# Kernel optimization log

Measured on AMD Instinct MI355X. Metric: run time of the kernel, lower is better.

The kernel has to match this reference:

```python
import jax, jax.numpy as jnp
import numpy as np


def setup_inputs() -> dict:
    key = jax.random.key(0)
    k1, k2, k3, k4 = jax.random.split(key, 4)
    B, C, H, W = 8, 3, 1024, 2048
    M, h, w = 32, H // 8, W // 8
    img = jax.random.uniform(k1, (B, C, H, W), dtype=jnp.float32)
    planar_masks = jax.random.normal(k2, (B, M, h, w), dtype=jnp.float32)
    disp = jax.random.uniform(k3, (B, h, w), dtype=jnp.float32) * 0.9 + 0.1
    K = jnp.array([[721.5, 0.0, w / 2.0], [0.0, 721.5, h / 2.0], [0.0, 0.0, 1.0]], dtype=jnp.float32)
    intrs = jnp.tile(K[None], (B, 1, 1))
    baseline = jax.random.uniform(k4, (B,), dtype=jnp.float32) * 0.4 + 0.3
    return {"img": img, "planar_masks": planar_masks, "disp": disp, "intrs": intrs, "baseline": baseline}


def reference(img, planar_masks, disp, intrs, baseline):
    B, C, H, W = img.shape
    _, M, h, w = planar_masks.shape
    dt = img.dtype

    # disp -> depth (b,h,w)
    focal = (intrs[:, 0, 0] + intrs[:, 1, 1]) * 0.5
    depth = baseline[:, None, None] * focal[:, None, None] / (disp * 2048.0)

    # depth -> normals via 3x3 Sobel-style central differences, zero padding
    dp = jnp.pad(depth, ((0, 0), (1, 1), (1, 1)))
    gx = 0.5 * (dp[:, 1:-1, 2:] - dp[:, 1:-1, :-2])
    gy = 0.5 * (dp[:, 2:, 1:-1] - dp[:, :-2, 1:-1])
    dir_map = jnp.stack([-gx, -gy, jnp.ones_like(gx)], axis=1)  # (B,3,h,w)
    normal = dir_map / jnp.sqrt(jnp.sum(dir_map ** 2, axis=1, keepdims=True))

    # softmax-weighted per-plane depth/normal (faithful torch .view memory layout)
    wts = jax.nn.softmax(planar_masks.reshape(B, M, h * w), axis=-1)  # (B,M,hw)
    flat_depth = depth.reshape(B, h * w, 1)
    flat_normal = normal.reshape(B, h * w, 3)  # channel-major flatten, as in source
    planar_depth = wts @ flat_depth   # (B,M,1)
    planar_normal = wts @ flat_normal  # (B,M,3)

    # per-plane homographies H = K (R - t n^T / d) K^-1
    R = jnp.broadcast_to(jnp.eye(3, dtype=dt), (B, 3, 3))
    t = jnp.zeros((B, 3, 1), dt).at[:, 2, 0].set(-baseline)
    K_inv = jnp.linalg.inv(intrs)
    tn = t[:, None] @ planar_normal[:, :, None, :]            # (B,M,3,3)
    H_cal = R[:, None] - tn / planar_depth[..., None]
    Hm = intrs[:, None] @ H_cal @ K_inv[:, None]              # (B,M,3,3)

    img_p = img.reshape(B, C, h, 8, w, 8).mean(axis=(3, 5))  # (B,C,h,w)

    # affine_grid (align_corners=True) with the top 2 rows of H
    ys = jnp.linspace(-1.0, 1.0, h, dtype=dt)
    xs = jnp.linspace(-1.0, 1.0, w, dtype=dt)
    gyy, gxx = jnp.meshgrid(ys, xs, indexing="ij")
    base = jnp.stack([gxx, gyy, jnp.ones_like(gxx)], axis=-1)  # (h,w,3)
    grid = jnp.einsum("bmij,hwj->bmhwi", Hm[:, :, :2, :], base)  # (B,M,h,w,2)

    # bilinear grid_sample, zeros padding, align_corners=True
    ix = (grid[..., 0] + 1.0) * (w - 1) * 0.5
    iy = (grid[..., 1] + 1.0) * (h - 1) * 0.5
    x0 = jnp.floor(ix)
    y0 = jnp.floor(iy)
    wx1 = ix - x0
    wy1 = iy - y0
    imgT = img_p.transpose(0, 2, 3, 1)  # (B,h,w,C)
    bidx = jnp.arange(B)[:, None, None, None]

    def corner(xf, yf):
        valid = (xf >= 0) & (xf <= w - 1) & (yf >= 0) & (yf <= h - 1)
        xi = jnp.clip(xf, 0, w - 1).astype(jnp.int32)
        yi = jnp.clip(yf, 0, h - 1).astype(jnp.int32)
        return imgT[bidx, yi, xi] * valid[..., None].astype(dt)  # (B,M,h,w,C)

    warp = (corner(x0, y0) * ((1 - wx1) * (1 - wy1))[..., None]
            + corner(x0 + 1, y0) * (wx1 * (1 - wy1))[..., None]
            + corner(x0, y0 + 1) * ((1 - wx1) * wy1)[..., None]
            + corner(x0 + 1, y0 + 1) * (wx1 * wy1)[..., None])  # (B,M,h,w,C)

    blend = jax.nn.softmax(planar_masks, axis=1)  # (B,M,h,w)
    return jnp.einsum("bmhwc,bmhw->bchw", warp, blend)
```

## Files before the change

kernel.cpp:

```cpp
#include <hip/hip_runtime.h>
#include <math.h>

#define Bq   8
#define Cc   3
#define Hh   128
#define Ww   256
#define Mm   32
#define HW   (Hh*Ww)
#define HIMG 1024
#define WIMG 2048

__global__ void k_pool_dn(const float* __restrict__ img,
                          float4* __restrict__ img_p,
                          const float* __restrict__ disp,
                          const float* __restrict__ intrs,
                          const float* __restrict__ baseline,
                          float* __restrict__ depth,
                          float* __restrict__ normal) {
    int blk = blockIdx.x;
    if (blk < Bq * Hh) {
        int b = blk >> 7, y = blk & (Hh - 1);
        int x = threadIdx.x;
        float s[3];
        #pragma unroll
        for (int c = 0; c < 3; c++) {
            const float* base = img + ((size_t)(b * 3 + c) * HIMG + (size_t)y * 8) * WIMG + x * 8;
            float acc = 0.f;
            #pragma unroll
            for (int r = 0; r < 8; r++) {
                float4 u = *(const float4*)(base + (size_t)r * WIMG);
                float4 v = *(const float4*)(base + (size_t)r * WIMG + 4);
                acc += u.x + u.y + u.z + u.w + v.x + v.y + v.z + v.w;
            }
            s[c] = acc * (1.0f / 64.0f);
        }
        img_p[(size_t)blk * Ww + x] = make_float4(s[0], s[1], s[2], 0.f);
    } else {
        int idx = (blk - Bq * Hh) * 256 + threadIdx.x;
        int b = idx >> 15;
        int p = idx & (HW - 1);
        int y = p >> 8;
        int x = p & (Ww - 1);
        float focal = 0.5f * (intrs[b * 9 + 0] + intrs[b * 9 + 4]);
        float k = baseline[b] * focal * (1.0f / 2048.0f);
        const float* db = disp + (size_t)b * HW;
        float Dc  = k / db[p];
        float Dxm = (x > 0)      ? k / db[p - 1]  : 0.0f;
        float Dxp = (x < Ww - 1) ? k / db[p + 1]  : 0.0f;
        float Dym = (y > 0)      ? k / db[p - Ww] : 0.0f;
        float Dyp = (y < Hh - 1) ? k / db[p + Ww] : 0.0f;
        float gx = 0.5f * (Dxp - Dxm);
        float gy = 0.5f * (Dyp - Dym);
        float invn = 1.0f / sqrtf(gx * gx + gy * gy + 1.0f);
        depth[idx] = Dc;
        float* nb = normal + (size_t)b * 3 * HW;
        nb[p]          = -gx * invn;
        nb[HW + p]     = -gy * invn;
        nb[2 * HW + p] =  invn;
    }
}

__global__ __launch_bounds__(1024) void k_planes(
        const float* __restrict__ masks,
        const float* __restrict__ depth,
        const float* __restrict__ normal,
        const float* __restrict__ intrs,
        const float* __restrict__ baseline,
        float* __restrict__ hm) {
    __shared__ float lds[5][16];
    int bm = blockIdx.x;
    int b = bm >> 5;
    const float4* mp = (const float4*)(masks + (size_t)bm * HW);
    const float4* dp = (const float4*)(depth + (size_t)b * HW);
    const float4* np = (const float4*)(normal + (size_t)b * 3 * HW);
    int tid = threadIdx.x;
    int lane = tid & 63, wid = tid >> 6;

    float se = 0.f, sd = 0.f, s0 = 0.f, s1 = 0.f, s2 = 0.f;
    #pragma unroll 4
    for (int kk = 0; kk < HW / 4 / 1024; kk++) {
        int i = tid + kk * 1024;
        float4 mk  = mp[i];
        float4 d4  = dp[i];
        float4 n0v = np[3 * i], n1v = np[3 * i + 1], n2v = np[3 * i + 2];
        float e0 = __expf(mk.x), e1 = __expf(mk.y);
        float e2 = __expf(mk.z), e3 = __expf(mk.w);
        se += (e0 + e1) + (e2 + e3);
        sd = fmaf(e0, d4.x, fmaf(e1, d4.y, fmaf(e2, d4.z, fmaf(e3, d4.w, sd))));
        s0 = fmaf(e0, n0v.x, fmaf(e1, n0v.w, fmaf(e2, n1v.z, fmaf(e3, n2v.y, s0))));
        s1 = fmaf(e0, n0v.y, fmaf(e1, n1v.x, fmaf(e2, n1v.w, fmaf(e3, n2v.z, s1))));
        s2 = fmaf(e0, n0v.z, fmaf(e1, n1v.y, fmaf(e2, n2v.x, fmaf(e3, n2v.w, s2))));
    }
    float vals[5] = {se, sd, s0, s1, s2};
    #pragma unroll
    for (int j = 0; j < 5; j++) {
        float v = vals[j];
        #pragma unroll
        for (int off = 32; off; off >>= 1) v += __shfl_down(v, off, 64);
        if (lane == 0) lds[j][wid] = v;
    }
    __syncthreads();

    if (tid == 0) {
        float t[5];
        #pragma unroll
        for (int j = 0; j < 5; j++) {
            float r = 0.f;
            #pragma unroll
            for (int i = 0; i < 16; i++) r += lds[j][i];
            t[j] = r;
        }
        float inv_se = 1.0f / t[0];
        float pd = t[1] * inv_se;
        float n0 = t[2] * inv_se, n1 = t[3] * inv_se, n2 = t[4] * inv_se;
        const float* Km = intrs + b * 9;
        float a = Km[0], bb = Km[1], c = Km[2];
        float d = Km[3], e  = Km[4], f = Km[5];
        float g = Km[6], h2 = Km[7], i = Km[8];
        float det = a * (e * i - f * h2) - bb * (d * i - f * g) + c * (d * h2 - e * g);
        float invd = 1.0f / det;
        float ki[9] = {(e * i - f * h2) * invd, (c * h2 - bb * i) * invd, (bb * f - c * e) * invd,
                       (f * g - d * i) * invd, (a * i - c * g) * invd,  (c * d - a * f) * invd,
                       (d * h2 - e * g) * invd, (bb * g - a * h2) * invd, (a * e - bb * d) * invd};
        float s = baseline[b] / pd;
        float A[9] = {1.f, 0.f, 0.f, 0.f, 1.f, 0.f, s * n0, s * n1, 1.0f + s * n2};
        float T[9];
        #pragma unroll
        for (int r = 0; r < 3; r++)
            #pragma unroll
            for (int cc = 0; cc < 3; cc++)
                T[r * 3 + cc] = Km[r * 3 + 0] * A[cc] + Km[r * 3 + 1] * A[3 + cc] + Km[r * 3 + 2] * A[6 + cc];
        #pragma unroll
        for (int r = 0; r < 2; r++)
            #pragma unroll
            for (int cc = 0; cc < 3; cc++)
                hm[bm * 6 + r * 3 + cc] = T[r * 3 + 0] * ki[cc] + T[r * 3 + 1] * ki[3 + cc] + T[r * 3 + 2] * ki[6 + cc];
    }
}

__global__ void k_blend(const float* __restrict__ masks,
                        const float* __restrict__ hm,
                        const float4* __restrict__ img_p,
                        float* __restrict__ out) {
    int bi = blockIdx.x;
    int b = bi >> 7;
    int y = bi & (Hh - 1);
    int x = threadIdx.x;
    __shared__ float hs[Mm * 6];
    if (x < Mm * 6) hs[x] = hm[b * Mm * 6 + x];
    __syncthreads();

    const float* mp = masks + (size_t)b * Mm * HW + (size_t)y * Ww + x;
    float mv[Mm];
    #pragma unroll
    for (int m = 0; m < Mm; m++) mv[m] = mp[(size_t)m * HW];

    float xn = (2.0f * x - (float)(Ww - 1)) * (1.0f / (float)(Ww - 1));
    float yn = (2.0f * y - (float)(Hh - 1)) * (1.0f / (float)(Hh - 1));
    const float4* ip = img_p + (size_t)b * HW;

    float se = 0.f, a0 = 0.f, a1 = 0.f, a2 = 0.f;
    #pragma unroll 4
    for (int m = 0; m < Mm; m++) {
        float e = __expf(mv[m]);
        se += e;
        float gx = fmaf(hs[m * 6 + 0], xn, fmaf(hs[m * 6 + 1], yn, hs[m * 6 + 2]));
        float gy = fmaf(hs[m * 6 + 3], xn, fmaf(hs[m * 6 + 4], yn, hs[m * 6 + 5]));
        float ix = (gx + 1.0f) * ((float)(Ww - 1) * 0.5f);
        float iy = (gy + 1.0f) * ((float)(Hh - 1) * 0.5f);
        float x0f = floorf(ix), y0f = floorf(iy);
        float wx1 = ix - x0f, wy1 = iy - y0f;
        float wx0 = 1.0f - wx1, wy0 = 1.0f - wy1;
        float w00 = wx0 * wy0 * e, w10 = wx1 * wy0 * e;
        float w01 = wx0 * wy1 * e, w11 = wx1 * wy1 * e;
        #define CORNER(xf, yf, wt) do {                                              \
            float _xf = (xf), _yf = (yf);                                            \
            bool _v = (_xf >= 0.0f) && (_xf <= (float)(Ww - 1)) &&                   \
                      (_yf >= 0.0f) && (_yf <= (float)(Hh - 1));                     \
            float _xc = fminf(fmaxf(_xf, 0.0f), (float)(Ww - 1));                    \
            float _yc = fminf(fmaxf(_yf, 0.0f), (float)(Hh - 1));                    \
            int _o = (int)_yc * Ww + (int)_xc;                                       \
            float4 _t = ip[_o];                                                      \
            float _w = _v ? (wt) : 0.0f;                                             \
            a0 = fmaf(_w, _t.x, a0);                                                 \
            a1 = fmaf(_w, _t.y, a1);                                                 \
            a2 = fmaf(_w, _t.z, a2);                                                 \
        } while (0)
        CORNER(x0f,        y0f,        w00);
        CORNER(x0f + 1.0f, y0f,        w10);
        CORNER(x0f,        y0f + 1.0f, w01);
        CORNER(x0f + 1.0f, y0f + 1.0f, w11);
        #undef CORNER
    }
    float inv = 1.0f / se;
    int o = y * Ww + x;
    float* ob = out + (size_t)b * 3 * HW;
    ob[o]          = a0 * inv;
    ob[HW + o]     = a1 * inv;
    ob[2 * HW + o] = a2 * inv;
}

extern "C" void kernel_launch(void* const* d_in, const int* in_sizes, int n_in,
                              void* d_out, int out_size, void* d_ws, size_t ws_size,
                              hipStream_t stream) {
    const float* img      = (const float*)d_in[0];
    const float* masks    = (const float*)d_in[1];
    const float* disp     = (const float*)d_in[2];
    const float* intrs    = (const float*)d_in[3];
    const float* baseline = (const float*)d_in[4];
    float* out = (float*)d_out;

    float* depth  = (float*)d_ws;
    float* normal = depth + (size_t)Bq * HW;
    float* hm     = normal + (size_t)Bq * 3 * HW;
    float4* img_p = (float4*)(hm + (size_t)Bq * Mm * 6);

    hipLaunchKernelGGL(k_pool_dn, dim3(2 * Bq * Hh), dim3(256), 0, stream,
                       img, img_p, disp, intrs, baseline, depth, normal);
    hipLaunchKernelGGL(k_planes, dim3(Bq * Mm), dim3(1024), 0, stream,
                       masks, depth, normal, intrs, baseline, hm);
    hipLaunchKernelGGL(k_blend, dim3(Bq * Hh), dim3(256), 0, stream,
                       masks, hm, img_p, out);
}
```

Before: 339.0 us.

## Overlap image pooling with plane reduction and split blend planes across two halves

Depth/normal computation moves into its own small kernel, and the large image pooling now runs in the same launch as the per-plane softmax reductions, so the two bandwidth-heavy phases can overlap instead of pooling sharing a launch with the tiny depth work. The plane reduction drops to 512 threads per block. The blend kernel uses 512 threads per row, with each half handling 16 of the 32 planes, and combines the partial sums through shared memory. This raises parallelism and lowers register pressure. The bilinear validity test is also simplified to per-axis unsigned compares. The cost is extra shared memory and a second sync in blend.

```diff
diff --git a/kernel.cpp b/kernel.cpp
--- a/kernel.cpp
+++ b/kernel.cpp
@@ -10,17 +10,116 @@
 #define HIMG 1024
 #define WIMG 2048
 
-__global__ void k_pool_dn(const float* __restrict__ img,
-                          float4* __restrict__ img_p,
-                          const float* __restrict__ disp,
-                          const float* __restrict__ intrs,
-                          const float* __restrict__ baseline,
-                          float* __restrict__ depth,
-                          float* __restrict__ normal) {
+__global__ void k_dn(const float* __restrict__ disp,
+                     const float* __restrict__ intrs,
+                     const float* __restrict__ baseline,
+                     float* __restrict__ depth,
+                     float* __restrict__ normal) {
+    int idx = blockIdx.x * 256 + threadIdx.x;
+    int b = idx >> 15;
+    int p = idx & (HW - 1);
+    int y = p >> 8;
+    int x = p & (Ww - 1);
+    float focal = 0.5f * (intrs[b * 9 + 0] + intrs[b * 9 + 4]);
+    float k = baseline[b] * focal * (1.0f / 2048.0f);
+    const float* db = disp + (size_t)b * HW;
+    float Dc  = k / db[p];
+    float Dxm = (x > 0)      ? k / db[p - 1]  : 0.0f;
+    float Dxp = (x < Ww - 1) ? k / db[p + 1]  : 0.0f;
+    float Dym = (y > 0)      ? k / db[p - Ww] : 0.0f;
+    float Dyp = (y < Hh - 1) ? k / db[p + Ww] : 0.0f;
+    float gx = 0.5f * (Dxp - Dxm);
+    float gy = 0.5f * (Dyp - Dym);
+    float invn = 1.0f / sqrtf(gx * gx + gy * gy + 1.0f);
+    depth[idx] = Dc;
+    float* nb = normal + (size_t)b * 3 * HW;
+    nb[p]          = -gx * invn;
+    nb[HW + p]     = -gy * invn;
+    nb[2 * HW + p] =  invn;
+}
+
+__global__ __launch_bounds__(512) void k_pool_planes(
+        const float* __restrict__ img, float4* __restrict__ img_p,
+        const float* __restrict__ masks,
+        const float* __restrict__ depth, const float* __restrict__ normal,
+        const float* __restrict__ intrs, const float* __restrict__ baseline,
+        float* __restrict__ hm) {
     int blk = blockIdx.x;
-    if (blk < Bq * Hh) {
-        int b = blk >> 7, y = blk & (Hh - 1);
-        int x = threadIdx.x;
+    int tid = threadIdx.x;
+    __shared__ float lds[5][8];
+    if (blk < Bq * Mm) {
+        int bm = blk;
+        int b = bm >> 5;
+        const float4* mp = (const float4*)(masks + (size_t)bm * HW);
+        const float4* dp = (const float4*)(depth + (size_t)b * HW);
+        const float4* np = (const float4*)(normal + (size_t)b * 3 * HW);
+        int lane = tid & 63, wid = tid >> 6;
+
+        float se = 0.f, sd = 0.f, s0 = 0.f, s1 = 0.f, s2 = 0.f;
+        #pragma unroll 4
+        for (int kk = 0; kk < HW / 4 / 512; kk++) {
+            int i = tid + kk * 512;
+            float4 mk  = mp[i];
+            float4 d4  = dp[i];
+            float4 n0v = np[3 * i], n1v = np[3 * i + 1], n2v = np[3 * i + 2];
+            float e0 = __expf(mk.x), e1 = __expf(mk.y);
+            float e2 = __expf(mk.z), e3 = __expf(mk.w);
+            se += (e0 + e1) + (e2 + e3);
+            sd = fmaf(e0, d4.x, fmaf(e1, d4.y, fmaf(e2, d4.z, fmaf(e3, d4.w, sd))));
+            s0 = fmaf(e0, n0v.x, fmaf(e1, n0v.w, fmaf(e2, n1v.z, fmaf(e3, n2v.y, s0))));
+            s1 = fmaf(e0, n0v.y, fmaf(e1, n1v.x, fmaf(e2, n1v.w, fmaf(e3, n2v.z, s1))));
+            s2 = fmaf(e0, n0v.z, fmaf(e1, n1v.y, fmaf(e2, n2v.x, fmaf(e3, n2v.w, s2))));
+        }
+        float vals[5] = {se, sd, s0, s1, s2};
+        #pragma unroll
+        for (int j = 0; j < 5; j++) {
+            float v = vals[j];
+            #pragma unroll
+            for (int off = 32; off; off >>= 1) v += __shfl_down(v, off, 64);
+            if (lane == 0) lds[j][wid] = v;
+        }
+        __syncthreads();
+
+        if (tid == 0) {
+            float t[5];
+            #pragma unroll
+            for (int j = 0; j < 5; j++) {
+                float r = 0.f;
+                #pragma unroll
+                for (int i = 0; i < 8; i++) r += lds[j][i];
+                t[j] = r;
+            }
+            float inv_se = 1.0f / t[0];
+            float pd = t[1] * inv_se;
+            float n0 = t[2] * inv_se, n1 = t[3] * inv_se, n2 = t[4] * inv_se;
+            const float* Km = intrs + b * 9;
+            float a = Km[0], bb = Km[1], c = Km[2];
+            float d = Km[3], e  = Km[4], f = Km[5];
+            float g = Km[6], h2 = Km[7], i = Km[8];
+            float det = a * (e * i - f * h2) - bb * (d * i - f * g) + c * (d * h2 - e * g);
+            float invd = 1.0f / det;
+            float ki[9] = {(e * i - f * h2) * invd, (c * h2 - bb * i) * invd, (bb * f - c * e) * invd,
+                           (f * g - d * i) * invd, (a * i - c * g) * invd,  (c * d - a * f) * invd,
+                           (d * h2 - e * g) * invd, (bb * g - a * h2) * invd, (a * e - bb * d) * invd};
+            float s = baseline[b] / pd;
+            float A[9] = {1.f, 0.f, 0.f, 0.f, 1.f, 0.f, s * n0, s * n1, 1.0f + s * n2};
+            float T[9];
+            #pragma unroll
+            for (int r = 0; r < 3; r++)
+                #pragma unroll
+                for (int cc = 0; cc < 3; cc++)
+                    T[r * 3 + cc] = Km[r * 3 + 0] * A[cc] + Km[r * 3 + 1] * A[3 + cc] + Km[r * 3 + 2] * A[6 + cc];
+            #pragma unroll
+            for (int r = 0; r < 2; r++)
+                #pragma unroll
+                for (int cc = 0; cc < 3; cc++)
+                    hm[bm * 6 + r * 3 + cc] = T[r * 3 + 0] * ki[cc] + T[r * 3 + 1] * ki[3 + cc] + T[r * 3 + 2] * ki[6 + cc];
+        }
+    } else {
+        int pb = blk - Bq * Mm;
+        int b = pb >> 6;
+        int y = ((pb & 63) << 1) | (tid >> 8);
+        int x = tid & 255;
         float s[3];
         #pragma unroll
         for (int c = 0; c < 3; c++) {
@@ -34,170 +133,80 @@
             }
             s[c] = acc * (1.0f / 64.0f);
         }
-        img_p[(size_t)blk * Ww + x] = make_float4(s[0], s[1], s[2], 0.f);
-    } else {
-        int idx = (blk - Bq * Hh) * 256 + threadIdx.x;
-        int b = idx >> 15;
-        int p = idx & (HW - 1);
-        int y = p >> 8;
-        int x = p & (Ww - 1);
-        float focal = 0.5f * (intrs[b * 9 + 0] + intrs[b * 9 + 4]);
-        float k = baseline[b] * focal * (1.0f / 2048.0f);
-        const float* db = disp + (size_t)b * HW;
-        float Dc  = k / db[p];
-        float Dxm = (x > 0)      ? k / db[p - 1]  : 0.0f;
-        float Dxp = (x < Ww - 1) ? k / db[p + 1]  : 0.0f;
-        float Dym = (y > 0)      ? k / db[p - Ww] : 0.0f;
-        float Dyp = (y < Hh - 1) ? k / db[p + Ww] : 0.0f;
-        float gx = 0.5f * (Dxp - Dxm);
-        float gy = 0.5f * (Dyp - Dym);
-        float invn = 1.0f / sqrtf(gx * gx + gy * gy + 1.0f);
-        depth[idx] = Dc;
-        float* nb = normal + (size_t)b * 3 * HW;
-        nb[p]          = -gx * invn;
-        nb[HW + p]     = -gy * invn;
-        nb[2 * HW + p] =  invn;
-    }
-}
-
-__global__ __launch_bounds__(1024) void k_planes(
-        const float* __restrict__ masks,
-        const float* __restrict__ depth,
-        const float* __restrict__ normal,
-        const float* __restrict__ intrs,
-        const float* __restrict__ baseline,
-        float* __restrict__ hm) {
-    __shared__ float lds[5][16];
-    int bm = blockIdx.x;
-    int b = bm >> 5;
-    const float4* mp = (const float4*)(masks + (size_t)bm * HW);
-    const float4* dp = (const float4*)(depth + (size_t)b * HW);
-    const float4* np = (const float4*)(normal + (size_t)b * 3 * HW);
-    int tid = threadIdx.x;
-    int lane = tid & 63, wid = tid >> 6;
-
-    float se = 0.f, sd = 0.f, s0 = 0.f, s1 = 0.f, s2 = 0.f;
-    #pragma unroll 4
-    for (int kk = 0; kk < HW / 4 / 1024; kk++) {
-        int i = tid + kk * 1024;
-        float4 mk  = mp[i];
-        float4 d4  = dp[i];
-        float4 n0v = np[3 * i], n1v = np[3 * i + 1], n2v = np[3 * i + 2];
-        float e0 = __expf(mk.x), e1 = __expf(mk.y);
-        float e2 = __expf(mk.z), e3 = __expf(mk.w);
-        se += (e0 + e1) + (e2 + e3);
-        sd = fmaf(e0, d4.x, fmaf(e1, d4.y, fmaf(e2, d4.z, fmaf(e3, d4.w, sd))));
-        s0 = fmaf(e0, n0v.x, fmaf(e1, n0v.w, fmaf(e2, n1v.z, fmaf(e3, n2v.y, s0))));
-        s1 = fmaf(e0, n0v.y, fmaf(e1, n1v.x, fmaf(e2, n1v.w, fmaf(e3, n2v.z, s1))));
-        s2 = fmaf(e0, n0v.z, fmaf(e1, n1v.y, fmaf(e2, n2v.x, fmaf(e3, n2v.w, s2))));
-    }
-    float vals[5] = {se, sd, s0, s1, s2};
-    #pragma unroll
-    for (int j = 0; j < 5; j++) {
-        float v = vals[j];
-        #pragma unroll
-        for (int off = 32; off; off >>= 1) v += __shfl_down(v, off, 64);
-        if (lane == 0) lds[j][wid] = v;
-    }
-    __syncthreads();
-
-    if (tid == 0) {
-        float t[5];
-        #pragma unroll
-        for (int j = 0; j < 5; j++) {
-            float r = 0.f;
-            #pragma unroll
-            for (int i = 0; i < 16; i++) r += lds[j][i];
-            t[j] = r;
-        }
-        float inv_se = 1.0f / t[0];
-        float pd = t[1] * inv_se;
-        float n0 = t[2] * inv_se, n1 = t[3] * inv_se, n2 = t[4] * inv_se;
-        const float* Km = intrs + b * 9;
-        float a = Km[0], bb = Km[1], c = Km[2];
-        float d = Km[3], e  = Km[4], f = Km[5];
-        float g = Km[6], h2 = Km[7], i = Km[8];
-        float det = a * (e * i - f * h2) - bb * (d * i - f * g) + c * (d * h2 - e * g);
-        float invd = 1.0f / det;
-        float ki[9] = {(e * i - f * h2) * invd, (c * h2 - bb * i) * invd, (bb * f - c * e) * invd,
-                       (f * g - d * i) * invd, (a * i - c * g) * invd,  (c * d - a * f) * invd,
-                       (d * h2 - e * g) * invd, (bb * g - a * h2) * invd, (a * e - bb * d) * invd};
-        float s = baseline[b] / pd;
-        float A[9] = {1.f, 0.f, 0.f, 0.f, 1.f, 0.f, s * n0, s * n1, 1.0f + s * n2};
-        float T[9];
-        #pragma unroll
-        for (int r = 0; r < 3; r++)
-            #pragma unroll
-            for (int cc = 0; cc < 3; cc++)
-                T[r * 3 + cc] = Km[r * 3 + 0] * A[cc] + Km[r * 3 + 1] * A[3 + cc] + Km[r * 3 + 2] * A[6 + cc];
-        #pragma unroll
-        for (int r = 0; r < 2; r++)
-            #pragma unroll
-            for (int cc = 0; cc < 3; cc++)
-                hm[bm * 6 + r * 3 + cc] = T[r * 3 + 0] * ki[cc] + T[r * 3 + 1] * ki[3 + cc] + T[r * 3 + 2] * ki[6 + cc];
-    }
-}
-
-__global__ void k_blend(const float* __restrict__ masks,
+        img_p[((size_t)(b * Hh + y)) * Ww + x] = make_float4(s[0], s[1], s[2], 0.f);
+    }
+}
+
+__global__ __launch_bounds__(512) void k_blend(const float* __restrict__ masks,
                         const float* __restrict__ hm,
                         const float4* __restrict__ img_p,
                         float* __restrict__ out) {
     int bi = blockIdx.x;
     int b = bi >> 7;
     int y = bi & (Hh - 1);
-    int x = threadIdx.x;
+    int tid = threadIdx.x;
+    int x = tid & (Ww - 1);
+    int half = tid >> 8;
     __shared__ float hs[Mm * 6];
-    if (x < Mm * 6) hs[x] = hm[b * Mm * 6 + x];
+    __shared__ float part[4][Ww];
+    if (tid < Mm * 6) hs[tid] = hm[b * Mm * 6 + tid];
     __syncthreads();
 
-    const float* mp = masks + (size_t)b * Mm * HW + (size_t)y * Ww + x;
-    float mv[Mm];
+    const float* mp = masks + (size_t)b * Mm * HW + (size_t)(half * 16) * HW
+                    + (size_t)y * Ww + x;
+    float mv[16];
     #pragma unroll
-    for (int m = 0; m < Mm; m++) mv[m] = mp[(size_t)m * HW];
+    for (int m = 0; m < 16; m++) mv[m] = mp[(size_t)m * HW];
 
     float xn = (2.0f * x - (float)(Ww - 1)) * (1.0f / (float)(Ww - 1));
     float yn = (2.0f * y - (float)(Hh - 1)) * (1.0f / (float)(Hh - 1));
     const float4* ip = img_p + (size_t)b * HW;
+    const float* hb = hs + half * 16 * 6;
 
     float se = 0.f, a0 = 0.f, a1 = 0.f, a2 = 0.f;
     #pragma unroll 4
-    for (int m = 0; m < Mm; m++) {
+    for (int m = 0; m < 16; m++) {
         float e = __expf(mv[m]);
         se += e;
-        float gx = fmaf(hs[m * 6 + 0], xn, fmaf(hs[m * 6 + 1], yn, hs[m * 6 + 2]));
-        float gy = fmaf(hs[m * 6 + 3], xn, fmaf(hs[m * 6 + 4], yn, hs[m * 6 + 5]));
+        float gx = fmaf(hb[m * 6 + 0], xn, fmaf(hb[m * 6 + 1], yn, hb[m * 6 + 2]));
+        float gy = fmaf(hb[m * 6 + 3], xn, fmaf(hb[m * 6 + 4], yn, hb[m * 6 + 5]));
         float ix = (gx + 1.0f) * ((float)(Ww - 1) * 0.5f);
         float iy = (gy + 1.0f) * ((float)(Hh - 1) * 0.5f);
         float x0f = floorf(ix), y0f = floorf(iy);
         float wx1 = ix - x0f, wy1 = iy - y0f;
         float wx0 = 1.0f - wx1, wy0 = 1.0f - wy1;
-        float w00 = wx0 * wy0 * e, w10 = wx1 * wy0 * e;
-        float w01 = wx0 * wy1 * e, w11 = wx1 * wy1 * e;
-        #define CORNER(xf, yf, wt) do {                                              \
-            float _xf = (xf), _yf = (yf);                                            \
-            bool _v = (_xf >= 0.0f) && (_xf <= (float)(Ww - 1)) &&                   \
-                      (_yf >= 0.0f) && (_yf <= (float)(Hh - 1));                     \
-            float _xc = fminf(fmaxf(_xf, 0.0f), (float)(Ww - 1));                    \
-            float _yc = fminf(fmaxf(_yf, 0.0f), (float)(Hh - 1));                    \
-            int _o = (int)_yc * Ww + (int)_xc;                                       \
-            float4 _t = ip[_o];                                                      \
-            float _w = _v ? (wt) : 0.0f;                                             \
-            a0 = fmaf(_w, _t.x, a0);                                                 \
-            a1 = fmaf(_w, _t.y, a1);                                                 \
-            a2 = fmaf(_w, _t.z, a2);                                                 \
-        } while (0)
-        CORNER(x0f,        y0f,        w00);
-        CORNER(x0f + 1.0f, y0f,        w10);
-        CORNER(x0f,        y0f + 1.0f, w01);
-        CORNER(x0f + 1.0f, y0f + 1.0f, w11);
-        #undef CORNER
-    }
-    float inv = 1.0f / se;
-    int o = y * Ww + x;
-    float* ob = out + (size_t)b * 3 * HW;
-    ob[o]          = a0 * inv;
-    ob[HW + o]     = a1 * inv;
-    ob[2 * HW + o] = a2 * inv;
+        int x0i = (int)x0f, y0i = (int)y0f;
+        float vx0 = ((unsigned)x0i       < (unsigned)Ww) ? wx0 : 0.0f;
+        float vx1 = ((unsigned)(x0i + 1) < (unsigned)Ww) ? wx1 : 0.0f;
+        float vy0 = ((unsigned)y0i       < (unsigned)Hh) ? wy0 * e : 0.0f;
+        float vy1 = ((unsigned)(y0i + 1) < (unsigned)Hh) ? wy1 * e : 0.0f;
+        int xc0 = min(max(x0i, 0), Ww - 1);
+        int xc1 = min(max(x0i + 1, 0), Ww - 1);
+        int r0 = min(max(y0i, 0), Hh - 1) * Ww;
+        int r1 = min(max(y0i + 1, 0), Hh - 1) * Ww;
+        float4 t00 = ip[r0 + xc0];
+        float4 t10 = ip[r0 + xc1];
+        float4 t01 = ip[r1 + xc0];
+        float4 t11 = ip[r1 + xc1];
+        float w00 = vx0 * vy0, w10 = vx1 * vy0;
+        float w01 = vx0 * vy1, w11 = vx1 * vy1;
+        a0 = fmaf(w00, t00.x, fmaf(w10, t10.x, fmaf(w01, t01.x, fmaf(w11, t11.x, a0))));
+        a1 = fmaf(w00, t00.y, fmaf(w10, t10.y, fmaf(w01, t01.y, fmaf(w11, t11.y, a1))));
+        a2 = fmaf(w00, t00.z, fmaf(w10, t10.z, fmaf(w01, t01.z, fmaf(w11, t11.z, a2))));
+    }
+    if (half) {
+        part[0][x] = se; part[1][x] = a0; part[2][x] = a1; part[3][x] = a2;
+    }
+    __syncthreads();
+    if (!half) {
+        se += part[0][x]; a0 += part[1][x]; a1 += part[2][x]; a2 += part[3][x];
+        float inv = 1.0f / se;
+        int o = y * Ww + x;
+        float* ob = out + (size_t)b * 3 * HW;
+        ob[o]          = a0 * inv;
+        ob[HW + o]     = a1 * inv;
+        ob[2 * HW + o] = a2 * inv;
+    }
 }
 
 extern "C" void kernel_launch(void* const* d_in, const int* in_sizes, int n_in,
@@ -215,10 +224,10 @@
     float* hm     = normal + (size_t)Bq * 3 * HW;
     float4* img_p = (float4*)(hm + (size_t)Bq * Mm * 6);
 
-    hipLaunchKernelGGL(k_pool_dn, dim3(2 * Bq * Hh), dim3(256), 0, stream,
-                       img, img_p, disp, intrs, baseline, depth, normal);
-    hipLaunchKernelGGL(k_planes, dim3(Bq * Mm), dim3(1024), 0, stream,
-                       masks, depth, normal, intrs, baseline, hm);
-    hipLaunchKernelGGL(k_blend, dim3(Bq * Hh), dim3(256), 0, stream,
+    hipLaunchKernelGGL(k_dn, dim3(Bq * Hh), dim3(256), 0, stream,
+                       disp, intrs, baseline, depth, normal);
+    hipLaunchKernelGGL(k_pool_planes, dim3(Bq * Mm + Bq * Hh / 2), dim3(512), 0, stream,
+                       img, img_p, masks, depth, normal, intrs, baseline, hm);
+    hipLaunchKernelGGL(k_blend, dim3(Bq * Hh), dim3(512), 0, stream,
                        masks, hm, img_p, out);
 }
```

After: 335.1 us. About the same (-1.2%).
